# Kernel tuning notes

Hardware: AMD Instinct MI355X
Metric: run time of the kernel (lower is better)

Reference implementation:

```python
import jax, jax.numpy as jnp
import numpy as np

N_NODES = 100000
N_EDGES = 800000
H_DIM = 128
E_DIM = 32
N_LAYER = 3


def setup_inputs() -> dict:
    key = jax.random.key(0)
    ks = jax.random.split(key, 5)
    x = jax.random.normal(ks[0], (N_NODES, H_DIM), dtype=jnp.float32)
    edge_index = jax.random.randint(ks[1], (2, N_EDGES), 0, N_NODES, dtype=jnp.int64)
    edge_attr = jax.random.normal(ks[2], (N_EDGES, E_DIM), dtype=jnp.float32)
    fan_in = 2 * H_DIM + E_DIM
    # torch Linear weight layout: [out_features, in_features]
    Wm = jax.random.normal(ks[3], (N_LAYER, H_DIM, fan_in), dtype=jnp.float32) / jnp.sqrt(fan_in)
    bm = jax.random.normal(ks[4], (N_LAYER, H_DIM), dtype=jnp.float32) * 0.01
    return {"x": x, "edge_index": edge_index, "edge_attr": edge_attr, "Wm": Wm, "bm": bm}


def reference(x, edge_index, edge_attr, Wm, bm):
    # PyG flow='source_to_target': row 0 = source (j), row 1 = target (i)
    src = edge_index[0]
    dst = edge_index[1]
    n_nodes = x.shape[0]
    n_layer = Wm.shape[0]
    for l in range(n_layer):  # small fixed layer count
        # message: m_ij = Linear(cat[x_j, x_i, edge_attr])
        m = jnp.concatenate([x[src], x[dst], edge_attr], axis=1)  # [E, 2h+e]
        m = jnp.einsum('ef,hf->eh', m, Wm[l]) + bm[l]             # [E, h]
        # aggr='add': scatter-add messages to target nodes
        x = jax.ops.segment_sum(m, dst, num_segments=n_nodes)     # [N, h]
        x = jax.nn.leaky_relu(x, negative_slope=0.01)
    # residual_connection='none' -> no-op; activate_last=True
    x = jax.nn.leaky_relu(x, negative_slope=0.01)
    return x
```

## Files before the change

kernel.cpp:

```cpp
#include <hip/hip_runtime.h>

#define N_NODES 100000
#define NP      100096
#define N_EDGES 800000
#define HD 128
#define ED 32
#define FAN 288
#define NL 3

#define SCHUNK 2048
#define SBLK   ((N_NODES + SCHUNK - 1) / SCHUNK)

#define TM 32
#define NTILES (NP / TM)
#define PGRID  1536

typedef short bf16x8 __attribute__((ext_vector_type(8)));
typedef short bf16x4 __attribute__((ext_vector_type(4)));
typedef float f32x4  __attribute__((ext_vector_type(4)));

__device__ inline float b2f(short s) {
    unsigned u = ((unsigned)(unsigned short)s) << 16;
    return __builtin_bit_cast(float, u);
}
__device__ inline short f2b(float f) {
    unsigned u = __builtin_bit_cast(unsigned, f);
    unsigned r = u + 0x7FFFu + ((u >> 16) & 1u);
    return (short)(r >> 16);
}


__global__ void count_kernel(const int* __restrict__ dst, int* __restrict__ deg) {
    int e = blockIdx.x * 256 + threadIdx.x;
    if (e < N_EDGES) atomicAdd(&deg[dst[e]], 1);
}

__global__ void scan_reduce(const int* __restrict__ deg, int* __restrict__ bsum) {
    __shared__ int ws[4];
    const int tid = threadIdx.x;
    int i0 = blockIdx.x * SCHUNK + tid * 8;
    int t = 0;
    #pragma unroll
    for (int j = 0; j < 8; ++j) {
        int i = i0 + j;
        if (i < N_NODES) t += deg[i];
    }
    #pragma unroll
    for (int off = 32; off >= 1; off >>= 1) t += __shfl_down(t, off, 64);
    if ((tid & 63) == 0) ws[tid >> 6] = t;
    __syncthreads();
    if (tid == 0) bsum[blockIdx.x] = ws[0] + ws[1] + ws[2] + ws[3];
}

__global__ void scan_final(const int* __restrict__ deg, const int* __restrict__ bsum,
                           int* __restrict__ ptr, int* __restrict__ cursor) {
    __shared__ int wsum[4];
    __shared__ int s_boff;
    const int tid = threadIdx.x;
    const int lane = tid & 63, wid = tid >> 6;
    if (wid == 0) {
        int v = (lane < SBLK) ? bsum[lane] : 0;
        int s = v;
        #pragma unroll
        for (int off = 1; off < 64; off <<= 1) {
            int t = __shfl_up(s, off, 64);
            if (lane >= off) s += t;
        }
        int srcl = (blockIdx.x == 0) ? 0 : (int)blockIdx.x - 1;
        int bprev = __shfl(s, srcl, 64);
        if (lane == 0) s_boff = (blockIdx.x == 0) ? 0 : bprev;
        int total = __shfl(s, SBLK - 1, 64);
        if (blockIdx.x == 0 && lane == 0) ptr[N_NODES] = total;
    }
    __syncthreads();

    int i0 = blockIdx.x * SCHUNK + tid * 8;
    int v[8]; int tsum = 0;
    #pragma unroll
    for (int j = 0; j < 8; ++j) {
        int i = i0 + j;
        v[j] = (i < N_NODES) ? deg[i] : 0;
        tsum += v[j];
    }
    int s = tsum;
    #pragma unroll
    for (int off = 1; off < 64; off <<= 1) {
        int t = __shfl_up(s, off, 64);
        if (lane >= off) s += t;
    }
    if (lane == 63) wsum[wid] = s;
    __syncthreads();
    int woff = 0;
    #pragma unroll
    for (int w = 0; w < 4; ++w) if (w < wid) woff += wsum[w];
    int excl = s_boff + woff + (s - tsum);
    #pragma unroll
    for (int j = 0; j < 8; ++j) {
        int i = i0 + j;
        if (i < N_NODES) { ptr[i] = excl; cursor[i] = excl; }
        excl += v[j];
    }
}

__global__ void fill_kernel(const int* __restrict__ src, const int* __restrict__ dst,
                            int* __restrict__ cursor, int2* __restrict__ csr2) {
    int e = blockIdx.x * 256 + threadIdx.x;
    if (e < N_EDGES) {
        int d = dst[e];
        int slot = atomicAdd(&cursor[d], 1);
        csr2[slot] = make_int2(src[e], e);
    }
}

__global__ void edge_sum(const int2* __restrict__ csr2, const int* __restrict__ ptr,
                         const float* __restrict__ eattr,
                         short* __restrict__ agge, float* __restrict__ degf) {
    int node = blockIdx.x * 32 + (threadIdx.x >> 3);
    int g = threadIdx.x & 7;
    if (node >= N_NODES) return;
    int s0 = ptr[node], s1 = ptr[node + 1];
    float4 a0 = make_float4(0.f,0.f,0.f,0.f), a1 = make_float4(0.f,0.f,0.f,0.f);
    int s = s0;
    int e0 = (s     < s1) ? csr2[s].y     : 0;
    int e1 = (s + 1 < s1) ? csr2[s + 1].y : 0;
    int e2 = (s + 2 < s1) ? csr2[s + 2].y : 0;
    int e3 = (s + 3 < s1) ? csr2[s + 3].y : 0;
    while (s + 4 <= s1) {
        float4 v0 = *reinterpret_cast<const float4*>(eattr + (size_t)e0 * ED + g * 4);
        float4 v1 = *reinterpret_cast<const float4*>(eattr + (size_t)e1 * ED + g * 4);
        float4 v2 = *reinterpret_cast<const float4*>(eattr + (size_t)e2 * ED + g * 4);
        float4 v3 = *reinterpret_cast<const float4*>(eattr + (size_t)e3 * ED + g * 4);
        s += 4;
        e0 = (s     < s1) ? csr2[s].y     : 0;
        e1 = (s + 1 < s1) ? csr2[s + 1].y : 0;
        e2 = (s + 2 < s1) ? csr2[s + 2].y : 0;
        e3 = (s + 3 < s1) ? csr2[s + 3].y : 0;
        a0.x += v0.x; a0.y += v0.y; a0.z += v0.z; a0.w += v0.w;
        a1.x += v1.x; a1.y += v1.y; a1.z += v1.z; a1.w += v1.w;
        a0.x += v2.x; a0.y += v2.y; a0.z += v2.z; a0.w += v2.w;
        a1.x += v3.x; a1.y += v3.y; a1.z += v3.z; a1.w += v3.w;
    }
    int rem = s1 - s;
    if (rem > 0) {
        float4 v = *reinterpret_cast<const float4*>(eattr + (size_t)e0 * ED + g * 4);
        a0.x += v.x; a0.y += v.y; a0.z += v.z; a0.w += v.w;
    }
    if (rem > 1) {
        float4 v = *reinterpret_cast<const float4*>(eattr + (size_t)e1 * ED + g * 4);
        a1.x += v.x; a1.y += v.y; a1.z += v.z; a1.w += v.w;
    }
    if (rem > 2) {
        float4 v = *reinterpret_cast<const float4*>(eattr + (size_t)e2 * ED + g * 4);
        a0.x += v.x; a0.y += v.y; a0.z += v.z; a0.w += v.w;
    }
    bf16x4 o;
    o[0] = f2b(a0.x + a1.x); o[1] = f2b(a0.y + a1.y);
    o[2] = f2b(a0.z + a1.z); o[3] = f2b(a0.w + a1.w);
    *reinterpret_cast<bf16x4*>(agge + (size_t)node * ED + g * 4) = o;
    if (g == 0) degf[node] = (float)(s1 - s0);
}

#define NW4 (NL * HD * FAN / 4)
#define NX4 (N_NODES * (HD / 4))
__global__ void conv_kernel(const float* __restrict__ Wm, short* __restrict__ Wb,
                            const float* __restrict__ x, short* __restrict__ xb) {
    int i4 = blockIdx.x * 256 + threadIdx.x;
    if (i4 < NW4) {
        float4 v = reinterpret_cast<const float4*>(Wm)[i4];
        bf16x4 o;
        o[0] = f2b(v.x); o[1] = f2b(v.y); o[2] = f2b(v.z); o[3] = f2b(v.w);
        reinterpret_cast<bf16x4*>(Wb)[i4] = o;
    }
    int j4 = i4 - NW4;
    if (j4 >= 0 && j4 < NX4) {
        float4 v = reinterpret_cast<const float4*>(x)[j4];
        bf16x4 o;
        o[0] = f2b(v.x); o[1] = f2b(v.y); o[2] = f2b(v.z); o[3] = f2b(v.w);
        reinterpret_cast<bf16x4*>(xb)[j4] = o;
    }
}

__global__ __launch_bounds__(256, 6) void fused_layer(
    const int* __restrict__ ptr, const int2* __restrict__ csr2,
    const short* __restrict__ xprev,
    const short* __restrict__ agge,
    const float* __restrict__ degf,
    const short* __restrict__ Wb,
    const float* __restrict__ b,
    float* __restrict__ out_f32,
    short* __restrict__ out_x,
    int* __restrict__ tick,
    int last)
{
    __shared__ char As[TM * 256];
    __shared__ int s_tile;
    const int tid = threadIdx.x;

    for (;;) {
        if (tid == 0) s_tile = atomicAdd(tick, 1);
        __syncthreads();
        const int tile = s_tile;
        if (tile >= NTILES) return;
        const int m0 = tile * TM;

        {
            const int ng = tid >> 4, g = tid & 15;
            #pragma unroll
            for (int i = 0; i < 2; ++i) {
                int row = i * 16 + ng;
                int node = m0 + row;
                float acc0[8] = {}, acc1[8] = {};
                if (node < N_NODES) {
                    int s0 = ptr[node], s1 = ptr[node + 1];
                    int s = s0;
                    int id[6];
                    #pragma unroll
                    for (int q = 0; q < 6; ++q) id[q] = (s + q < s1) ? csr2[s + q].x : 0;
                    while (s + 6 <= s1) {
                        bf16x8 v[6];
                        #pragma unroll
                        for (int q = 0; q < 6; ++q)
                            v[q] = *reinterpret_cast<const bf16x8*>(
                                xprev + (size_t)id[q] * HD + g * 8);
                        s += 6;
                        #pragma unroll
                        for (int q = 0; q < 6; ++q) id[q] = (s + q < s1) ? csr2[s + q].x : 0;
                        #pragma unroll
                        for (int q = 0; q < 6; ++q) {
                            float* ac = (q & 1) ? acc1 : acc0;
                            #pragma unroll
                            for (int j = 0; j < 8; ++j) ac[j] += b2f(v[q][j]);
                        }
                    }
                    int rem = s1 - s;
                    #pragma unroll
                    for (int q = 0; q < 5; ++q) {
                        if (q < rem) {
                            bf16x8 v = *reinterpret_cast<const bf16x8*>(
                                xprev + (size_t)id[q] * HD + g * 8);
                            float* ac = (q & 1) ? acc1 : acc0;
                            #pragma unroll
                            for (int j = 0; j < 8; ++j) ac[j] += b2f(v[j]);
                        }
                    }
                }
                bf16x8 o;
                #pragma unroll
                for (int j = 0; j < 8; ++j) o[j] = f2b(acc0[j] + acc1[j]);
                int byte = row * 256 + g * 16;
                byte ^= (row & 7) << 4;
                *reinterpret_cast<bf16x8*>(As + byte) = o;
            }
        }
        __syncthreads();

        const int w = tid >> 6, lane = tid & 63;
        const int l15 = lane & 15, lq = lane >> 4;
        const int kb = lq * 8;

        f32x4 acc1[2][2], acc2[2][2];
        #pragma unroll
        for (int i = 0; i < 2; ++i)
            #pragma unroll
            for (int j = 0; j < 2; ++j) {
                acc1[i][j] = (f32x4){0.f, 0.f, 0.f, 0.f};
                acc2[i][j] = (f32x4){0.f, 0.f, 0.f, 0.f};
            }

        #pragma unroll
        for (int kt = 0; kt < 4; ++kt) {
            bf16x8 a[2], bf[2];
            #pragma unroll
            for (int mf = 0; mf < 2; ++mf) {
                int row = mf * 16 + l15;
                int byte = row * 256 + kt * 64 + kb * 2;
                byte ^= (row & 7) << 4;
                a[mf] = *reinterpret_cast<const bf16x8*>(As + byte);
            }
            #pragma unroll
            for (int nf = 0; nf < 2; ++nf) {
                int c = w * 32 + nf * 16 + l15;
                bf[nf] = *reinterpret_cast<const bf16x8*>(Wb + (size_t)c * FAN + kt * 32 + kb);
            }
            #pragma unroll
            for (int mf = 0; mf < 2; ++mf)
                #pragma unroll
                for (int nf = 0; nf < 2; ++nf)
                    acc1[mf][nf] = __builtin_amdgcn_mfma_f32_16x16x32_bf16(
                        a[mf], bf[nf], acc1[mf][nf], 0, 0, 0);
        }
        #pragma unroll
        for (int kt = 4; kt < 9; ++kt) {
            bf16x8 a[2], bf[2];
            #pragma unroll
            for (int mf = 0; mf < 2; ++mf) {
                size_t arow = (size_t)(m0 + mf * 16 + l15);
                a[mf] = (kt < 8)
                    ? *reinterpret_cast<const bf16x8*>(xprev + arow * HD + (kt * 32 - 128) + kb)
                    : *reinterpret_cast<const bf16x8*>(agge + arow * ED + kb);
            }
            #pragma unroll
            for (int nf = 0; nf < 2; ++nf) {
                int c = w * 32 + nf * 16 + l15;
                bf[nf] = *reinterpret_cast<const bf16x8*>(Wb + (size_t)c * FAN + kt * 32 + kb);
            }
            #pragma unroll
            for (int mf = 0; mf < 2; ++mf)
                #pragma unroll
                for (int nf = 0; nf < 2; ++nf) {
                    if (kt < 8)
                        acc2[mf][nf] = __builtin_amdgcn_mfma_f32_16x16x32_bf16(
                            a[mf], bf[nf], acc2[mf][nf], 0, 0, 0);
                    else
                        acc1[mf][nf] = __builtin_amdgcn_mfma_f32_16x16x32_bf16(
                            a[mf], bf[nf], acc1[mf][nf], 0, 0, 0);
                }
        }

        #pragma unroll
        for (int mf = 0; mf < 2; ++mf) {
            int r0 = m0 + mf * 16 + lq * 4;
            float dg[4];
            #pragma unroll
            for (int j = 0; j < 4; ++j)
                dg[j] = (r0 + j < N_NODES) ? degf[r0 + j] : 0.f;
            #pragma unroll
            for (int nf = 0; nf < 2; ++nf) {
                int c = w * 32 + nf * 16 + l15;
                float bc = b[c];
                #pragma unroll
                for (int j = 0; j < 4; ++j) {
                    int row = r0 + j;
                    if (row >= N_NODES) continue;
                    float v = acc1[mf][nf][j] + dg[j] * (acc2[mf][nf][j] + bc);
                    v = (v >= 0.f) ? v : 0.01f * v;
                    if (last) {
                        v = (v >= 0.f) ? v : 0.01f * v;
                        out_f32[(size_t)row * HD + c] = v;
                    } else {
                        out_x[(size_t)row * HD + c] = f2b(v);
                    }
                }
            }
        }
    }
}

extern "C" void kernel_launch(void* const* d_in, const int* in_sizes, int n_in,
                              void* d_out, int out_size, void* d_ws, size_t ws_size,
                              hipStream_t stream) {
    const float* x_in  = (const float*)d_in[0];
    const int*   ei    = (const int*)d_in[1];
    const float* eattr = (const float*)d_in[2];
    const float* Wm    = (const float*)d_in[3];
    const float* bm    = (const float*)d_in[4];
    float* out = (float*)d_out;

    char* ws = (char*)d_ws;
    size_t off = 0;
    auto alloc = [&](size_t bytes) -> void* {
        void* p = ws + off;
        off = (off + bytes + 255) & ~(size_t)255;
        return p;
    };
    short* x0      = (short*)alloc((size_t)NP * HD * 2);
    short* x1      = (short*)alloc((size_t)NP * HD * 2);
    short* agge    = (short*)alloc((size_t)NP * ED * 2);
    float* degf    = (float*)alloc((size_t)NP * 4);
    int*   deg     = (int*)alloc((size_t)N_NODES * 4);
    int*   tickets = (int*)alloc(256);
    int*   ptr     = (int*)alloc((size_t)(N_NODES + 1) * 4);
    int*   cursor  = (int*)alloc((size_t)N_NODES * 4);
    int2*  csr2    = (int2*)alloc((size_t)N_EDGES * 8);
    short* Wb      = (short*)alloc((size_t)NL * HD * FAN * 2);
    int*   bsum    = (int*)alloc((size_t)SBLK * 4);

    const int* src = ei;
    const int* dst = ei + N_EDGES;

    hipMemsetAsync(deg, 0, (size_t)((char*)tickets - (char*)deg) + 64, stream);
    count_kernel<<<(N_EDGES + 255) / 256, 256, 0, stream>>>(dst, deg);
    scan_reduce<<<SBLK, 256, 0, stream>>>(deg, bsum);
    scan_final<<<SBLK, 256, 0, stream>>>(deg, bsum, ptr, cursor);
    fill_kernel<<<(N_EDGES + 255) / 256, 256, 0, stream>>>(src, dst, cursor, csr2);
    edge_sum<<<(N_NODES + 31) / 32, 256, 0, stream>>>(csr2, ptr, eattr, agge, degf);
    conv_kernel<<<(NW4 + NX4 + 255) / 256, 256, 0, stream>>>(Wm, Wb, x_in, x0);

    short* xping[2] = {x0, x1};
    for (int l = 0; l < NL; ++l) {
        fused_layer<<<PGRID, 256, 0, stream>>>(
            ptr, csr2, xping[l & 1], agge, degf,
            Wb + (size_t)l * HD * FAN, bm + (size_t)l * HD,
            out, xping[(l + 1) & 1], tickets + l, (l == NL - 1) ? 1 : 0);
    }
}
```

Baseline: 424.6 us.

## Replace persistent atomic tile scheduler with one block per tile

The fused layer kernel drops its persistent-grid design, where blocks pulled tiles through an atomic ticket counter, and launches one block per 32-node tile instead. This removes the per-tile atomic and the extra barrier, and the ticket buffer and its memset go away. It also drops the occupancy hint in launch bounds and cuts the gather unroll from 6 to 4 neighbours, which lowers register pressure but exposes less memory-level parallelism per thread. It now relies on the hardware dispatcher for load balancing across tiles with uneven degree.

```diff
diff --git a/kernel.cpp b/kernel.cpp
--- a/kernel.cpp
+++ b/kernel.cpp
@@ -12,8 +12,6 @@
 #define SBLK   ((N_NODES + SCHUNK - 1) / SCHUNK)
 
 #define TM 32
-#define NTILES (NP / TM)
-#define PGRID  1536
 
 typedef short bf16x8 __attribute__((ext_vector_type(8)));
 typedef short bf16x4 __attribute__((ext_vector_type(4)));
@@ -180,7 +178,7 @@
     }
 }
 
-__global__ __launch_bounds__(256, 6) void fused_layer(
+__global__ __launch_bounds__(256) void fused_layer(
     const int* __restrict__ ptr, const int2* __restrict__ csr2,
     const short* __restrict__ xprev,
     const short* __restrict__ agge,
@@ -189,157 +187,157 @@
     const float* __restrict__ b,
     float* __restrict__ out_f32,
     short* __restrict__ out_x,
-    int* __restrict__ tick,
     int last)
 {
     __shared__ char As[TM * 256];
-    __shared__ int s_tile;
     const int tid = threadIdx.x;
-
-    for (;;) {
-        if (tid == 0) s_tile = atomicAdd(tick, 1);
-        __syncthreads();
-        const int tile = s_tile;
-        if (tile >= NTILES) return;
-        const int m0 = tile * TM;
-
-        {
-            const int ng = tid >> 4, g = tid & 15;
+    const int m0 = blockIdx.x * TM;
+
+    {
+        const int ng = tid >> 4, g = tid & 15;
+        #pragma unroll
+        for (int i = 0; i < 2; ++i) {
+            int row = i * 16 + ng;
+            int node = m0 + row;
+            float acc0[8] = {}, acc1[8] = {};
+            if (node < N_NODES) {
+                int s0 = ptr[node], s1 = ptr[node + 1];
+                int s = s0;
+                int i0 = (s     < s1) ? csr2[s].x     : 0;
+                int i1 = (s + 1 < s1) ? csr2[s + 1].x : 0;
+                int i2 = (s + 2 < s1) ? csr2[s + 2].x : 0;
+                int i3 = (s + 3 < s1) ? csr2[s + 3].x : 0;
+                while (s + 4 <= s1) {
+                    bf16x8 v0 = *reinterpret_cast<const bf16x8*>(xprev + (size_t)i0 * HD + g * 8);
+                    bf16x8 v1 = *reinterpret_cast<const bf16x8*>(xprev + (size_t)i1 * HD + g * 8);
+                    bf16x8 v2 = *reinterpret_cast<const bf16x8*>(xprev + (size_t)i2 * HD + g * 8);
+                    bf16x8 v3 = *reinterpret_cast<const bf16x8*>(xprev + (size_t)i3 * HD + g * 8);
+                    s += 4;
+                    i0 = (s     < s1) ? csr2[s].x     : 0;
+                    i1 = (s + 1 < s1) ? csr2[s + 1].x : 0;
+                    i2 = (s + 2 < s1) ? csr2[s + 2].x : 0;
+                    i3 = (s + 3 < s1) ? csr2[s + 3].x : 0;
+                    #pragma unroll
+                    for (int j = 0; j < 8; ++j) acc0[j] += b2f(v0[j]);
+                    #pragma unroll
+                    for (int j = 0; j < 8; ++j) acc1[j] += b2f(v1[j]);
+                    #pragma unroll
+                    for (int j = 0; j < 8; ++j) acc0[j] += b2f(v2[j]);
+                    #pragma unroll
+                    for (int j = 0; j < 8; ++j) acc1[j] += b2f(v3[j]);
+                }
+                int rem = s1 - s;
+                if (rem > 0) {
+                    bf16x8 v = *reinterpret_cast<const bf16x8*>(xprev + (size_t)i0 * HD + g * 8);
+                    #pragma unroll
+                    for (int j = 0; j < 8; ++j) acc0[j] += b2f(v[j]);
+                }
+                if (rem > 1) {
+                    bf16x8 v = *reinterpret_cast<const bf16x8*>(xprev + (size_t)i1 * HD + g * 8);
+                    #pragma unroll
+                    for (int j = 0; j < 8; ++j) acc1[j] += b2f(v[j]);
+                }
+                if (rem > 2) {
+                    bf16x8 v = *reinterpret_cast<const bf16x8*>(xprev + (size_t)i2 * HD + g * 8);
+                    #pragma unroll
+                    for (int j = 0; j < 8; ++j) acc0[j] += b2f(v[j]);
+                }
+            }
+            bf16x8 o;
             #pragma unroll
-            for (int i = 0; i < 2; ++i) {
-                int row = i * 16 + ng;
-                int node = m0 + row;
-                float acc0[8] = {}, acc1[8] = {};
-                if (node < N_NODES) {
-                    int s0 = ptr[node], s1 = ptr[node + 1];
-                    int s = s0;
-                    int id[6];
-                    #pragma unroll
-                    for (int q = 0; q < 6; ++q) id[q] = (s + q < s1) ? csr2[s + q].x : 0;
-                    while (s + 6 <= s1) {
-                        bf16x8 v[6];
-                        #pragma unroll
-                        for (int q = 0; q < 6; ++q)
-                            v[q] = *reinterpret_cast<const bf16x8*>(
-                                xprev + (size_t)id[q] * HD + g * 8);
-                        s += 6;
-                        #pragma unroll
-                        for (int q = 0; q < 6; ++q) id[q] = (s + q < s1) ? csr2[s + q].x : 0;
-                        #pragma unroll
-                        for (int q = 0; q < 6; ++q) {
-                            float* ac = (q & 1) ? acc1 : acc0;
-                            #pragma unroll
-                            for (int j = 0; j < 8; ++j) ac[j] += b2f(v[q][j]);
-                        }
-                    }
-                    int rem = s1 - s;
-                    #pragma unroll
-                    for (int q = 0; q < 5; ++q) {
-                        if (q < rem) {
-                            bf16x8 v = *reinterpret_cast<const bf16x8*>(
-                                xprev + (size_t)id[q] * HD + g * 8);
-                            float* ac = (q & 1) ? acc1 : acc0;
-                            #pragma unroll
-                            for (int j = 0; j < 8; ++j) ac[j] += b2f(v[j]);
-                        }
-                    }
-                }
-                bf16x8 o;
-                #pragma unroll
-                for (int j = 0; j < 8; ++j) o[j] = f2b(acc0[j] + acc1[j]);
-                int byte = row * 256 + g * 16;
-                byte ^= (row & 7) << 4;
-                *reinterpret_cast<bf16x8*>(As + byte) = o;
-            }
-        }
-        __syncthreads();
-
-        const int w = tid >> 6, lane = tid & 63;
-        const int l15 = lane & 15, lq = lane >> 4;
-        const int kb = lq * 8;
-
-        f32x4 acc1[2][2], acc2[2][2];
-        #pragma unroll
-        for (int i = 0; i < 2; ++i)
+            for (int j = 0; j < 8; ++j) o[j] = f2b(acc0[j] + acc1[j]);
+            int byte = row * 256 + g * 16;
+            byte ^= (row & 7) << 4;
+            *reinterpret_cast<bf16x8*>(As + byte) = o;
+        }
+    }
+    __syncthreads();
+
+    const int w = tid >> 6, lane = tid & 63;
+    const int l15 = lane & 15, lq = lane >> 4;
+    const int kb = lq * 8;
+
+    f32x4 acc1[2][2], acc2[2][2];
+    #pragma unroll
+    for (int i = 0; i < 2; ++i)
+        #pragma unroll
+        for (int j = 0; j < 2; ++j) {
+            acc1[i][j] = (f32x4){0.f, 0.f, 0.f, 0.f};
+            acc2[i][j] = (f32x4){0.f, 0.f, 0.f, 0.f};
+        }
+
+    #pragma unroll
+    for (int kt = 0; kt < 4; ++kt) {
+        bf16x8 a[2], bf[2];
+        #pragma unroll
+        for (int mf = 0; mf < 2; ++mf) {
+            int row = mf * 16 + l15;
+            int byte = row * 256 + kt * 64 + kb * 2;
+            byte ^= (row & 7) << 4;
+            a[mf] = *reinterpret_cast<const bf16x8*>(As + byte);
+        }
+        #pragma unroll
+        for (int nf = 0; nf < 2; ++nf) {
+            int c = w * 32 + nf * 16 + l15;
+            bf[nf] = *reinterpret_cast<const bf16x8*>(Wb + (size_t)c * FAN + kt * 32 + kb);
+        }
+        #pragma unroll
+        for (int mf = 0; mf < 2; ++mf)
             #pragma unroll
-            for (int j = 0; j < 2; ++j) {
-                acc1[i][j] = (f32x4){0.f, 0.f, 0.f, 0.f};
-                acc2[i][j] = (f32x4){0.f, 0.f, 0.f, 0.f};
-            }
-
-        #pragma unroll
-        for (int kt = 0; kt < 4; ++kt) {
-            bf16x8 a[2], bf[2];
-            #pragma unroll
-            for (int mf = 0; mf < 2; ++mf) {
-                int row = mf * 16 + l15;
-                int byte = row * 256 + kt * 64 + kb * 2;
-                byte ^= (row & 7) << 4;
-                a[mf] = *reinterpret_cast<const bf16x8*>(As + byte);
-            }
+            for (int nf = 0; nf < 2; ++nf)
+                acc1[mf][nf] = __builtin_amdgcn_mfma_f32_16x16x32_bf16(
+                    a[mf], bf[nf], acc1[mf][nf], 0, 0, 0);
+    }
+    #pragma unroll
+    for (int kt = 4; kt < 9; ++kt) {
+        bf16x8 a[2], bf[2];
+        #pragma unroll
+        for (int mf = 0; mf < 2; ++mf) {
+            size_t arow = (size_t)(m0 + mf * 16 + l15);
+            a[mf] = (kt < 8)
+                ? *reinterpret_cast<const bf16x8*>(xprev + arow * HD + (kt * 32 - 128) + kb)
+                : *reinterpret_cast<const bf16x8*>(agge + arow * ED + kb);
+        }
+        #pragma unroll
+        for (int nf = 0; nf < 2; ++nf) {
+            int c = w * 32 + nf * 16 + l15;
+            bf[nf] = *reinterpret_cast<const bf16x8*>(Wb + (size_t)c * FAN + kt * 32 + kb);
+        }
+        #pragma unroll
+        for (int mf = 0; mf < 2; ++mf)
             #pragma unroll
             for (int nf = 0; nf < 2; ++nf) {
-                int c = w * 32 + nf * 16 + l15;
-                bf[nf] = *reinterpret_cast<const bf16x8*>(Wb + (size_t)c * FAN + kt * 32 + kb);
-            }
-            #pragma unroll
-            for (int mf = 0; mf < 2; ++mf)
-                #pragma unroll
-                for (int nf = 0; nf < 2; ++nf)
+                if (kt < 8)
+                    acc2[mf][nf] = __builtin_amdgcn_mfma_f32_16x16x32_bf16(
+                        a[mf], bf[nf], acc2[mf][nf], 0, 0, 0);
+                else
                     acc1[mf][nf] = __builtin_amdgcn_mfma_f32_16x16x32_bf16(
                         a[mf], bf[nf], acc1[mf][nf], 0, 0, 0);
-        }
-        #pragma unroll
-        for (int kt = 4; kt < 9; ++kt) {
-            bf16x8 a[2], bf[2];
+            }
+    }
+
+    #pragma unroll
+    for (int mf = 0; mf < 2; ++mf) {
+        int r0 = m0 + mf * 16 + lq * 4;
+        float dg[4];
+        #pragma unroll
+        for (int j = 0; j < 4; ++j)
+            dg[j] = (r0 + j < N_NODES) ? degf[r0 + j] : 0.f;
+        #pragma unroll
+        for (int nf = 0; nf < 2; ++nf) {
+            int c = w * 32 + nf * 16 + l15;
+            float bc = b[c];
             #pragma unroll
-            for (int mf = 0; mf < 2; ++mf) {
-                size_t arow = (size_t)(m0 + mf * 16 + l15);
-                a[mf] = (kt < 8)
-                    ? *reinterpret_cast<const bf16x8*>(xprev + arow * HD + (kt * 32 - 128) + kb)
-                    : *reinterpret_cast<const bf16x8*>(agge + arow * ED + kb);
-            }
-            #pragma unroll
-            for (int nf = 0; nf < 2; ++nf) {
-                int c = w * 32 + nf * 16 + l15;
-                bf[nf] = *reinterpret_cast<const bf16x8*>(Wb + (size_t)c * FAN + kt * 32 + kb);
-            }
-            #pragma unroll
-            for (int mf = 0; mf < 2; ++mf)
-                #pragma unroll
-                for (int nf = 0; nf < 2; ++nf) {
-                    if (kt < 8)
-                        acc2[mf][nf] = __builtin_amdgcn_mfma_f32_16x16x32_bf16(
-                            a[mf], bf[nf], acc2[mf][nf], 0, 0, 0);
-                    else
-                        acc1[mf][nf] = __builtin_amdgcn_mfma_f32_16x16x32_bf16(
-                            a[mf], bf[nf], acc1[mf][nf], 0, 0, 0);
-                }
-        }
-
-        #pragma unroll
-        for (int mf = 0; mf < 2; ++mf) {
-            int r0 = m0 + mf * 16 + lq * 4;
-            float dg[4];
-            #pragma unroll
-            for (int j = 0; j < 4; ++j)
-                dg[j] = (r0 + j < N_NODES) ? degf[r0 + j] : 0.f;
-            #pragma unroll
-            for (int nf = 0; nf < 2; ++nf) {
-                int c = w * 32 + nf * 16 + l15;
-                float bc = b[c];
-                #pragma unroll
-                for (int j = 0; j < 4; ++j) {
-                    int row = r0 + j;
-                    if (row >= N_NODES) continue;
-                    float v = acc1[mf][nf][j] + dg[j] * (acc2[mf][nf][j] + bc);
+            for (int j = 0; j < 4; ++j) {
+                int row = r0 + j;
+                if (row >= N_NODES) continue;
+                float v = acc1[mf][nf][j] + dg[j] * (acc2[mf][nf][j] + bc);
+                v = (v >= 0.f) ? v : 0.01f * v;
+                if (last) {
                     v = (v >= 0.f) ? v : 0.01f * v;
-                    if (last) {
-                        v = (v >= 0.f) ? v : 0.01f * v;
-                        out_f32[(size_t)row * HD + c] = v;
-                    } else {
-                        out_x[(size_t)row * HD + c] = f2b(v);
-                    }
+                    out_f32[(size_t)row * HD + c] = v;
+                } else {
+                    out_x[(size_t)row * HD + c] = f2b(v);
                 }
             }
         }
@@ -368,7 +366,6 @@
     short* agge    = (short*)alloc((size_t)NP * ED * 2);
     float* degf    = (float*)alloc((size_t)NP * 4);
     int*   deg     = (int*)alloc((size_t)N_NODES * 4);
-    int*   tickets = (int*)alloc(256);
     int*   ptr     = (int*)alloc((size_t)(N_NODES + 1) * 4);
     int*   cursor  = (int*)alloc((size_t)N_NODES * 4);
     int2*  csr2    = (int2*)alloc((size_t)N_EDGES * 8);
@@ -378,7 +375,7 @@
     const int* src = ei;
     const int* dst = ei + N_EDGES;
 
-    hipMemsetAsync(deg, 0, (size_t)((char*)tickets - (char*)deg) + 64, stream);
+    hipMemsetAsync(deg, 0, (size_t)N_NODES * 4, stream);
     count_kernel<<<(N_EDGES + 255) / 256, 256, 0, stream>>>(dst, deg);
     scan_reduce<<<SBLK, 256, 0, stream>>>(deg, bsum);
     scan_final<<<SBLK, 256, 0, stream>>>(deg, bsum, ptr, cursor);
@@ -388,9 +385,9 @@
 
     short* xping[2] = {x0, x1};
     for (int l = 0; l < NL; ++l) {
-        fused_layer<<<PGRID, 256, 0, stream>>>(
+        fused_layer<<<NP / TM, 256, 0, stream>>>(
             ptr, csr2, xping[l & 1], agge, degf,
             Wb + (size_t)l * HD * FAN, bm + (size_t)l * HD,
-            out, xping[(l + 1) & 1], tickets + l, (l == NL - 1) ? 1 : 0);
-    }
-}
+            out, xping[(l + 1) & 1], (l == NL - 1) ? 1 : 0);
+    }
+}
```

Result: faster. 348.4 us (-18.0%).
